# Kernel tuning notes

Measured on AMD Instinct MI355X. Metric: run time of the kernel, lower is better.

The kernel has to match this reference:

```python
import jax, jax.numpy as jnp
import numpy as np

EPS = 1e-5
HEADS, KK, UU, VV, MM = 4, 16, 1, 64, 23
PAD = (MM - 1) // 2


def _bn(x, gamma, beta, mean, var):
    # eval-mode BatchNorm2d over channel axis 1 of (b, c, w, h)
    scale = gamma / jnp.sqrt(var + EPS)
    return (x - mean[:, None, None]) * scale[:, None, None] + beta[:, None, None]


def setup_inputs() -> dict:
    key = jax.random.key(0)
    ks = jax.random.split(key, 13)
    B, C, W, H = 8, 256, 64, 64
    return {
        "x": jax.random.normal(ks[0], (B, C, W, H), jnp.float32),
        "Wq": jax.random.normal(ks[1], (KK * HEADS, C), jnp.float32) * 0.05,
        "q_gamma": jax.random.uniform(ks[2], (KK * HEADS,), jnp.float32),
        "q_beta": jax.random.normal(ks[3], (KK * HEADS,), jnp.float32) * 0.05,
        "q_mean": jax.random.normal(ks[4], (KK * HEADS,), jnp.float32) * 0.05,
        "q_var": jax.random.uniform(ks[5], (KK * HEADS,), jnp.float32) + 0.5,
        "Wk": jax.random.normal(ks[6], (KK * UU, C), jnp.float32) * 0.05,
        "Wv": jax.random.normal(ks[7], (VV * UU, C), jnp.float32) * 0.05,
        "v_gamma": jax.random.uniform(ks[8], (VV * UU,), jnp.float32),
        "v_beta": jax.random.normal(ks[9], (VV * UU,), jnp.float32) * 0.05,
        "v_mean": jax.random.normal(ks[10], (VV * UU,), jnp.float32) * 0.05,
        "v_var": jax.random.uniform(ks[11], (VV * UU,), jnp.float32) + 0.5,
        "embedding": jax.random.normal(ks[12], (KK, UU, 1, MM, MM), jnp.float32),
    }


def reference(x, Wq, q_gamma, q_beta, q_mean, q_var, Wk, Wv, v_gamma, v_beta, v_mean, v_var, embedding):
    b, C, w, h = x.shape
    n = w * h
    # 1x1 conv projections as channel GEMMs
    q = jnp.einsum('bcij,oc->boij', x, Wq)
    q = _bn(q, q_gamma, q_beta, q_mean, q_var).reshape(b, HEADS, KK, n)
    kf = jnp.einsum('bcij,oc->boij', x, Wk).reshape(b, KK, UU, n)
    kf = jax.nn.softmax(kf, axis=-1)  # softmax over spatial positions
    v = jnp.einsum('bcij,oc->boij', x, Wv)
    v = _bn(v, v_gamma, v_beta, v_mean, v_var)  # (b, vv*uu, w, h)
    v_flat = v.reshape(b, VV, UU, n)
    # content lambda
    lambda_c = jnp.einsum('bkum,bvum->bkv', kf, v_flat)
    y_c = jnp.einsum('bhkn,bkv->bhvn', q, lambda_c)
    # positional lambda via depth-1 conv3d over (vv, w, h)
    v5 = v.reshape(b, UU, VV, w, h)
    lambda_p = jax.lax.conv_general_dilated(
        v5, embedding, window_strides=(1, 1, 1),
        padding=[(0, 0), (PAD, PAD), (PAD, PAD)],
        dimension_numbers=('NCDHW', 'OIDHW', 'NCDHW'))  # (b, kk, vv, w, h)
    lambda_p = lambda_p.reshape(b, KK, VV, n)
    y_p = jnp.einsum('bhkn,bkvn->bhvn', q, lambda_p)
    out = (y_c + y_p).reshape(b, HEADS * VV, w, h)
    return out
```

## Files before the change

kernel.cpp:

```cpp
#include <hip/hip_runtime.h>

typedef __attribute__((ext_vector_type(8))) short bf16x8;
typedef __attribute__((ext_vector_type(4))) float f32x4;

#define EPS 1e-5f
#define B 8
#define C 256
#define NPIX 4096
#define NCH 144
#define ROW_V 64
#define ROW_KF 128
#define PAD 11
#define VH_WORDS 3840

#define WP_OFF    0u
#define BIAS_OFF  36864u
#define PROJ_OFF  37120u
#define RMAX_OFF  4755712u
#define RSC_OFF   4755840u
#define LC_OFF    4755968u
#define ET_OFF    4764160u
#define QT_OFF    4811264u
#define OUTT_OFF  6908416u
#define WS_NEED_QT    6908416u
#define WS_NEED_FULL  15297024u

__device__ inline short f2bf(float f) {
  unsigned u = __float_as_uint(f);
  return (short)((u + 0x7fffu + ((u >> 16) & 1u)) >> 16);
}

__global__ __launch_bounds__(256) void k_wfold(
    const float* __restrict__ Wq, const float* __restrict__ qg, const float* __restrict__ qb,
    const float* __restrict__ qm, const float* __restrict__ qv,
    const float* __restrict__ Wk, const float* __restrict__ Wv,
    const float* __restrict__ vg, const float* __restrict__ vb,
    const float* __restrict__ vm, const float* __restrict__ vvar,
    float* __restrict__ Wt, float* __restrict__ biasp) {
  int o = blockIdx.x;
  int t = threadIdx.x;
  const float* src; float s, bias;
  if (o < 64) {
    s = qg[o] * rsqrtf(qv[o] + EPS); bias = qb[o] - qm[o] * s; src = Wq + o * C;
  } else if (o < 128) {
    int i = o - 64;
    s = vg[i] * rsqrtf(vvar[i] + EPS); bias = vb[i] - vm[i] * s; src = Wv + i * C;
  } else {
    int i = o - 128; s = 1.f; bias = 0.f; src = Wk + i * C;
  }
  Wt[t * NCH + o] = src[t] * s;
  if (t == 0) biasp[o] = bias;
}

__global__ __launch_bounds__(256) void k_wprep(
    const float* __restrict__ Wt, ushort* __restrict__ wtA) {
  int i = blockIdx.x * 256 + threadIdx.x;
  int mt = i >> 9;
  int rest = i & 511;
  int kt = rest >> 6;
  int lane = rest & 63;
  int m = mt * 16 + (lane & 15);
  int c0 = kt * 32 + (lane >> 4) * 8;
  ushort* dst = wtA + (size_t)i * 8;
  #pragma unroll
  for (int j = 0; j < 8; j++) {
    float v = Wt[(c0 + j) * NCH + m];
    unsigned u = __float_as_uint(v);
    dst[j] = (ushort)((u + 0x7fffu + ((u >> 16) & 1u)) >> 16);
  }
}

__global__ __launch_bounds__(256) void k_eprep(
    const float* __restrict__ emb, ushort* __restrict__ etw) {
  int i = blockIdx.x * 256 + threadIdx.x;
  int s = i / 11776;
  int r = i % 11776;
  int dy = r / 512;
  int l = (r / 8) % 64;
  int jj = r % 8;
  int f = l & 15, q = l >> 4;
  int dx = q * 8 + jj - s;
  float val = (dx >= 0 && dx < 23) ? emb[f * 529 + dy * 23 + dx] : 0.f;
  unsigned u = __float_as_uint(val);
  etw[i] = (ushort)((u + 0x7fffu + ((u >> 16) & 1u)) >> 16);
}

__global__ __launch_bounds__(256) void k_projm(
    const float* __restrict__ x, const ushort* __restrict__ wtA,
    const float* __restrict__ biasp, float* __restrict__ proj) {
  int ntile = blockIdx.x;
  int b = blockIdx.y;
  int t = threadIdx.x;
  int lane = t & 63, w = t >> 6;
  int px = ntile * 64 + w * 16 + (lane & 15);
  int kq = lane >> 4;
  const float* xb = x + (size_t)b * C * NPIX + px;
  const bf16x8* A = (const bf16x8*)wtA;
  f32x4 acc[9];
  #pragma unroll
  for (int i = 0; i < 9; i++) acc[i] = (f32x4)(0.f);
  #pragma unroll 2
  for (int kt = 0; kt < 8; kt++) {
    int c0 = kt * 32 + kq * 8;
    bf16x8 bb;
    #pragma unroll
    for (int j = 0; j < 8; j++) bb[j] = f2bf(xb[(size_t)(c0 + j) * NPIX]);
    #pragma unroll
    for (int mt = 0; mt < 9; mt++) {
      bf16x8 a = A[(mt * 8 + kt) * 64 + lane];
      acc[mt] = __builtin_amdgcn_mfma_f32_16x16x32_bf16(a, bb, acc[mt], 0, 0, 0);
    }
  }
  float* pb = proj + (size_t)b * NCH * NPIX + px;
  #pragma unroll
  for (int mt = 0; mt < 9; mt++) {
    #pragma unroll
    for (int r = 0; r < 4; r++) {
      int ch = mt * 16 + kq * 4 + r;
      pb[(size_t)ch * NPIX] = acc[mt][r] + biasp[ch];
    }
  }
}

__global__ __launch_bounds__(256) void k_proj(
    const float* __restrict__ x, const float* __restrict__ Wt,
    const float* __restrict__ biasp, float* __restrict__ proj) {
  int tile = blockIdx.x;
  int g = blockIdx.y;
  int b = blockIdx.z;
  int t = threadIdx.x;
  int px = tile * 256 + t;
  const float* xb = x + (size_t)b * C * NPIX + px;
  float acc[18];
  #pragma unroll
  for (int i = 0; i < 18; i++) acc[i] = 0.f;
  #pragma unroll 4
  for (int c = 0; c < C; c++) {
    float xv = xb[(size_t)c * NPIX];
    const float* wrow = Wt + c * NCH + g * 18;
    #pragma unroll
    for (int i = 0; i < 18; i++) acc[i] += xv * wrow[i];
  }
  float* ob = proj + ((size_t)b * NCH + g * 18) * NPIX + px;
  #pragma unroll
  for (int i = 0; i < 18; i++) ob[(size_t)i * NPIX] = acc[i] + biasp[g * 18 + i];
}

__global__ __launch_bounds__(256) void k_qtrans(
    const float* __restrict__ proj, float* __restrict__ qT) {
  int ch = blockIdx.x, b = blockIdx.y, t = threadIdx.x;
  __shared__ float buf[4608];
  const float* src = proj + ((size_t)b * NCH + ch) * NPIX;
  for (int it = 0; it < 16; it++) {
    int p = it * 256 + t;
    buf[p + (p >> 3)] = src[p];
  }
  __syncthreads();
  float* dst = qT + ((size_t)b * 64 + ch) * NPIX;
  for (int it = 0; it < 16; it++) {
    int idx = it * 256 + t;
    int s = idx >> 9, i = idx & 511;
    int p = (i >> 3) * 64 + (i & 7) * 8 + s;
    dst[idx] = buf[p + (p >> 3)];
  }
}

__global__ __launch_bounds__(256) void k_vhalo(
    const float* __restrict__ proj, uint* __restrict__ vhg) {
  int v = blockIdx.x, b = blockIdx.y, t = threadIdx.x;
  const float* vrow = proj + ((size_t)b * NCH + ROW_V + v) * NPIX;
  uint* dst = vhg + (size_t)b * NCH * NPIX + (size_t)v * VH_WORDS;
  for (int p2 = t; p2 < 3784; p2 += 256) {
    int hr = p2 / 44;
    int hc = (p2 % 44) * 2;
    int ir = hr - 11;
    int ic0 = hc - 11, ic1 = hc - 10;
    bool rok = (ir >= 0 && ir < 64);
    float f0 = (rok && ic0 >= 0 && ic0 < 64) ? vrow[ir * 64 + ic0] : 0.f;
    float f1 = (rok && ic1 >= 0 && ic1 < 64) ? vrow[ir * 64 + ic1] : 0.f;
    uint u0 = __float_as_uint(f0), u1 = __float_as_uint(f1);
    uint h0 = (u0 + 0x7fffu + ((u0 >> 16) & 1u)) >> 16;
    uint h1 = (u1 + 0x7fffu + ((u1 >> 16) & 1u)) >> 16;
    dst[p2] = (h0 & 0xffffu) | (h1 << 16);
  }
}

__global__ __launch_bounds__(256) void k_softstat(
    const float* __restrict__ proj, float* __restrict__ rmax, float* __restrict__ rsc) {
  int k = blockIdx.x, b = blockIdx.y, t = threadIdx.x;
  const float* row = proj + ((size_t)b * NCH + ROW_KF + k) * NPIX;
  __shared__ float sd[256];
  float m = -1e30f;
  for (int n = t; n < NPIX; n += 256) m = fmaxf(m, row[n]);
  sd[t] = m; __syncthreads();
  for (int s = 128; s > 0; s >>= 1) { if (t < s) sd[t] = fmaxf(sd[t], sd[t + s]); __syncthreads(); }
  m = sd[0]; __syncthreads();
  float sum = 0.f;
  for (int n = t; n < NPIX; n += 256) sum += __expf(row[n] - m);
  sd[t] = sum; __syncthreads();
  for (int s = 128; s > 0; s >>= 1) { if (t < s) sd[t] += sd[t + s]; __syncthreads(); }
  if (t == 0) { rmax[b * 16 + k] = m; rsc[b * 16 + k] = 1.f / sd[0]; }
}

__global__ __launch_bounds__(256) void k_lambda_c(
    const float* __restrict__ proj, const float* __restrict__ rmax,
    const float* __restrict__ rsc, float* __restrict__ lc) {
  int split = blockIdx.x;
  int b = blockIdx.y;
  int t = threadIdx.x;
  int lane = t & 63, w = t >> 6;
  int kr = lane & 15;
  int half = lane >> 4;
  float m = rmax[b * 16 + kr], sc = rsc[b * 16 + kr];
  const float* kfrow = proj + ((size_t)b * NCH + ROW_KF + kr) * NPIX;
  const float* vrow  = proj + ((size_t)b * NCH + ROW_V + w * 16 + kr) * NPIX;
  f32x4 acc = (f32x4)(0.f);
  #pragma unroll
  for (int c = 0; c < 2; c++) {
    int n0 = split * 64 + c * 32 + half * 8;
    float4 fa0 = *(const float4*)(kfrow + n0);
    float4 fa1 = *(const float4*)(kfrow + n0 + 4);
    float4 fb0 = *(const float4*)(vrow + n0);
    float4 fb1 = *(const float4*)(vrow + n0 + 4);
    bf16x8 a, bb;
    a[0] = f2bf(__expf(fa0.x - m) * sc); a[1] = f2bf(__expf(fa0.y - m) * sc);
    a[2] = f2bf(__expf(fa0.z - m) * sc); a[3] = f2bf(__expf(fa0.w - m) * sc);
    a[4] = f2bf(__expf(fa1.x - m) * sc); a[5] = f2bf(__expf(fa1.y - m) * sc);
    a[6] = f2bf(__expf(fa1.z - m) * sc); a[7] = f2bf(__expf(fa1.w - m) * sc);
    bb[0] = f2bf(fb0.x); bb[1] = f2bf(fb0.y); bb[2] = f2bf(fb0.z); bb[3] = f2bf(fb0.w);
    bb[4] = f2bf(fb1.x); bb[5] = f2bf(fb1.y); bb[6] = f2bf(fb1.z); bb[7] = f2bf(fb1.w);
    acc = __builtin_amdgcn_mfma_f32_16x16x32_bf16(a, bb, acc, 0, 0, 0);
  }
  #pragma unroll
  for (int r = 0; r < 4; r++) {
    int k = half * 4 + r;
    atomicAdd(&lc[((size_t)b * 16 + k) * 64 + w * 16 + kr], acc[r]);
  }
}

__global__ __launch_bounds__(256, 2) void k_conv_mfma(
    const float* __restrict__ proj, const ushort* __restrict__ etw,
    const float* __restrict__ qT, const float* __restrict__ lc,
    const uint* __restrict__ vhg,
    float* __restrict__ outT, float* __restrict__ out, int mode) {
  int s = blockIdx.x;
  int v = blockIdx.y;
  int b = blockIdx.z;
  int t = threadIdx.x;
  __shared__ __align__(16) ushort vh[86 * 88];
  __shared__ __align__(16) ushort elds[23 * 64 * 8];

  {
    const uint4* src = (const uint4*)etw + s * 1472;
    uint4* dst = (uint4*)elds;
    for (int i = t; i < 1472; i += 256) dst[i] = src[i];
  }
  if (mode != 0) {
    const uint4* vsrc = (const uint4*)(vhg + (size_t)b * NCH * NPIX + (size_t)v * VH_WORDS);
    uint4* vdst = (uint4*)vh;
    for (int i = t; i < 946; i += 256) vdst[i] = vsrc[i];
  } else {
    const float* vrow = proj + ((size_t)b * NCH + ROW_V + v) * NPIX;
    for (int i = t; i < 86 * 88; i += 256) {
      int hr = i / 88, hc = i % 88;
      int ir = hr - 11, ic = hc - 11;
      float val = (ir >= 0 && ir < 64 && ic >= 0 && ic < 64) ? vrow[ir * 64 + ic] : 0.f;
      unsigned u = __float_as_uint(val);
      vh[i] = (ushort)((u + 0x7fffu + ((u >> 16) & 1u)) >> 16);
    }
  }
  __syncthreads();

  int lane = t & 63, w = t >> 6;
  int n_ = lane & 15, q = lane >> 4;
  int rn = n_ >> 3, g = n_ & 7;

  f32x4 acc[8];
  #pragma unroll
  for (int i = 0; i < 8; i++) acc[i] = (f32x4)(0.f);

  const bf16x8* vh8 = (const bf16x8*)vh;
  const bf16x8* e8 = (const bf16x8*)elds;
  int baseA = (w * 16 + rn) * 11 + g + q;

  bf16x8 bfr[16];
  #pragma unroll
  for (int r = 0; r < 16; r++)
    bfr[(r & 1) * 8 + ((r >> 1) & 7)] = vh8[baseA + r * 11];

  #pragma unroll
  for (int dy = 0; dy < 23; dy++) {
    bf16x8 ef = e8[dy * 64 + lane];
    bf16x8 tmp;
    if (dy + 16 <= 36) tmp = vh8[baseA + (dy + 16) * 11];
    #pragma unroll
    for (int tt = 0; tt < 8; tt++) {
      int r = dy + 2 * tt;
      acc[tt] = __builtin_amdgcn_mfma_f32_16x16x32_bf16(
          ef, bfr[(r & 1) * 8 + ((r >> 1) & 7)], acc[tt], 0, 0, 0);
    }
    if (dy + 16 <= 36) {
      int rr = dy + 16;
      bfr[(rr & 1) * 8 + ((rr >> 1) & 7)] = tmp;
    }
  }

  float lcv[4];
  #pragma unroll
  for (int r = 0; r < 4; r++) lcv[r] = lc[((size_t)b * 16 + q * 4 + r) * 64 + v];

  if (mode != 0) {
    const float* qTb = qT + (size_t)b * 64 * NPIX;
    float* obT = outT + (size_t)b * 256 * NPIX;
    float* ob = out + (size_t)b * 256 * NPIX;
    #pragma unroll
    for (int tt = 0; tt < 8; tt++) {
      int row = w * 16 + 2 * tt + rn;
      int io = s * 512 + row * 8 + g;
      float lam[4];
      #pragma unroll
      for (int r = 0; r < 4; r++) lam[r] = acc[tt][r] + lcv[r];
      float y[4];
      #pragma unroll
      for (int h = 0; h < 4; h++) {
        float a = 0.f;
        #pragma unroll
        for (int r = 0; r < 4; r++)
          a += qTb[(size_t)(h * 16 + q * 4 + r) * NPIX + io] * lam[r];
        y[h] = a;
      }
      #pragma unroll
      for (int h = 0; h < 4; h++) {
        y[h] += __shfl_xor(y[h], 16);
        y[h] += __shfl_xor(y[h], 32);
      }
      if (q == 0) {
        if (mode == 2) {
          #pragma unroll
          for (int h = 0; h < 4; h++) obT[(size_t)(h * 64 + v) * NPIX + io] = y[h];
        } else {
          int p = row * 64 + 8 * g + s;
          #pragma unroll
          for (int h = 0; h < 4; h++) ob[(size_t)(h * 64 + v) * NPIX + p] = y[h];
        }
      }
    }
  } else {
    const float* qbp = proj + (size_t)b * NCH * NPIX;
    float* ob = out + (size_t)b * 256 * NPIX;
    #pragma unroll
    for (int tt = 0; tt < 8; tt++) {
      int p = (w * 16 + 2 * tt + rn) * 64 + 8 * g + s;
      float lam[4];
      #pragma unroll
      for (int r = 0; r < 4; r++) lam[r] = acc[tt][r] + lcv[r];
      float y[4];
      #pragma unroll
      for (int h = 0; h < 4; h++) {
        float a = 0.f;
        #pragma unroll
        for (int r = 0; r < 4; r++)
          a += qbp[(size_t)(h * 16 + q * 4 + r) * NPIX + p] * lam[r];
        y[h] = a;
      }
      #pragma unroll
      for (int h = 0; h < 4; h++) {
        y[h] += __shfl_xor(y[h], 16);
        y[h] += __shfl_xor(y[h], 32);
      }
      if (q == 0) {
        #pragma unroll
        for (int h = 0; h < 4; h++) ob[(size_t)(h * 64 + v) * NPIX + p] = y[h];
      }
    }
  }
}

__global__ __launch_bounds__(256) void k_outtrans(
    const float* __restrict__ outT, float* __restrict__ out) {
  int ch = blockIdx.x, b = blockIdx.y, t = threadIdx.x;
  __shared__ float buf[4608];
  const float* src = outT + ((size_t)b * 256 + ch) * NPIX;
  for (int it = 0; it < 16; it++) {
    int idx = it * 256 + t;
    int s = idx >> 9, i = idx & 511;
    int p = (i >> 3) * 64 + (i & 7) * 8 + s;
    buf[p + (p >> 3)] = src[idx];
  }
  __syncthreads();
  float* dst = out + ((size_t)b * 256 + ch) * NPIX;
  for (int it = 0; it < 16; it++) {
    int p = it * 256 + t;
    dst[p] = buf[p + (p >> 3)];
  }
}

extern "C" void kernel_launch(void* const* d_in, const int* in_sizes, int n_in,
                              void* d_out, int out_size, void* d_ws, size_t ws_size,
                              hipStream_t stream) {
  const float* x    = (const float*)d_in[0];
  const float* Wq   = (const float*)d_in[1];
  const float* qg   = (const float*)d_in[2];
  const float* qbta = (const float*)d_in[3];
  const float* qm   = (const float*)d_in[4];
  const float* qv   = (const float*)d_in[5];
  const float* Wk   = (const float*)d_in[6];
  const float* Wv   = (const float*)d_in[7];
  const float* vg   = (const float*)d_in[8];
  const float* vb   = (const float*)d_in[9];
  const float* vm   = (const float*)d_in[10];
  const float* vvar = (const float*)d_in[11];
  const float* emb  = (const float*)d_in[12];
  float* ws   = (float*)d_ws;
  float* Wt   = ws + WP_OFF;
  float* bp   = ws + BIAS_OFF;
  float* proj = ws + PROJ_OFF;
  float* rmax = ws + RMAX_OFF;
  float* rsc  = ws + RSC_OFF;
  float* lcw  = ws + LC_OFF;
  ushort* etw = (ushort*)(ws + ET_OFF);
  float* qT   = ws + QT_OFF;
  float* outT = ws + OUTT_OFF;
  float* out  = (float*)d_out;
  uint* vhg   = (uint*)proj;
  ushort* wtA = (ushort*)qT;

  size_t wsf = ws_size / sizeof(float);
  int mode = (wsf >= WS_NEED_FULL) ? 2 : ((wsf >= WS_NEED_QT) ? 1 : 0);

  hipLaunchKernelGGL(k_wfold, dim3(144), dim3(256), 0, stream,
                     Wq, qg, qbta, qm, qv, Wk, Wv, vg, vb, vm, vvar, Wt, bp);
  hipLaunchKernelGGL(k_eprep, dim3(368), dim3(256), 0, stream, emb, etw);
  hipMemsetAsync(lcw, 0, 16 * 64 * B * sizeof(float), stream);
  if (mode >= 1) {
    hipLaunchKernelGGL(k_wprep, dim3(18), dim3(256), 0, stream, Wt, wtA);
    hipLaunchKernelGGL(k_projm, dim3(64, 8), dim3(256), 0, stream, x, wtA, bp, proj);
    hipLaunchKernelGGL(k_qtrans, dim3(64, 8), dim3(256), 0, stream, proj, qT);
    hipLaunchKernelGGL(k_vhalo, dim3(64, 8), dim3(256), 0, stream, proj, vhg);
  } else {
    hipLaunchKernelGGL(k_proj, dim3(16, 8, 8), dim3(256), 0, stream, x, Wt, bp, proj);
  }
  hipLaunchKernelGGL(k_softstat, dim3(16, 8), dim3(256), 0, stream, proj, rmax, rsc);
  hipLaunchKernelGGL(k_lambda_c, dim3(64, 8), dim3(256), 0, stream, proj, rmax, rsc, lcw);
  hipLaunchKernelGGL(k_conv_mfma, dim3(8, 64, 8), dim3(256), 0, stream,
                     proj, etw, qT, lcw, vhg, outT, out, mode);
  if (mode == 2)
    hipLaunchKernelGGL(k_outtrans, dim3(256, 8), dim3(256), 0, stream, outT, out);
}
```

Before: 217.1 us.

## Fuse softmax stats into lambda_c, merge prep kernels, read embedding from global

Drops the separate softmax-statistics kernel. The unnormalized exp is accumulated into lambda_c along with a per-row sum via atomics, and the conv kernel divides by that sum. The weight-fold and embedding-prep kernels are merged into one launch. The conv kernel now reads embedding fragments directly from global memory instead of staging them in LDS, and its occupancy hint is raised to 6. Skipping max-subtraction risks exp overflow for large logits, and the global embedding reads depend on cache hits.

```diff
diff --git a/kernel.cpp b/kernel.cpp
--- a/kernel.cpp
+++ b/kernel.cpp
@@ -17,7 +17,6 @@
 #define BIAS_OFF  36864u
 #define PROJ_OFF  37120u
 #define RMAX_OFF  4755712u
-#define RSC_OFF   4755840u
 #define LC_OFF    4755968u
 #define ET_OFF    4764160u
 #define QT_OFF    4811264u
@@ -30,26 +29,41 @@
   return (short)((u + 0x7fffu + ((u >> 16) & 1u)) >> 16);
 }
 
-__global__ __launch_bounds__(256) void k_wfold(
+__global__ __launch_bounds__(256) void k_prep(
     const float* __restrict__ Wq, const float* __restrict__ qg, const float* __restrict__ qb,
     const float* __restrict__ qm, const float* __restrict__ qv,
     const float* __restrict__ Wk, const float* __restrict__ Wv,
     const float* __restrict__ vg, const float* __restrict__ vb,
     const float* __restrict__ vm, const float* __restrict__ vvar,
-    float* __restrict__ Wt, float* __restrict__ biasp) {
-  int o = blockIdx.x;
+    const float* __restrict__ emb,
+    float* __restrict__ Wt, float* __restrict__ biasp, ushort* __restrict__ etw) {
   int t = threadIdx.x;
-  const float* src; float s, bias;
-  if (o < 64) {
-    s = qg[o] * rsqrtf(qv[o] + EPS); bias = qb[o] - qm[o] * s; src = Wq + o * C;
-  } else if (o < 128) {
-    int i = o - 64;
-    s = vg[i] * rsqrtf(vvar[i] + EPS); bias = vb[i] - vm[i] * s; src = Wv + i * C;
+  if (blockIdx.x < 144) {
+    int o = blockIdx.x;
+    const float* src; float s, bias;
+    if (o < 64) {
+      s = qg[o] * rsqrtf(qv[o] + EPS); bias = qb[o] - qm[o] * s; src = Wq + o * C;
+    } else if (o < 128) {
+      int i = o - 64;
+      s = vg[i] * rsqrtf(vvar[i] + EPS); bias = vb[i] - vm[i] * s; src = Wv + i * C;
+    } else {
+      int i = o - 128; s = 1.f; bias = 0.f; src = Wk + i * C;
+    }
+    Wt[t * NCH + o] = src[t] * s;
+    if (t == 0) biasp[o] = bias;
   } else {
-    int i = o - 128; s = 1.f; bias = 0.f; src = Wk + i * C;
-  }
-  Wt[t * NCH + o] = src[t] * s;
-  if (t == 0) biasp[o] = bias;
+    int i = (blockIdx.x - 144) * 256 + t;
+    int s = i / 11776;
+    int r = i % 11776;
+    int dy = r / 512;
+    int l = (r / 8) % 64;
+    int jj = r % 8;
+    int f = l & 15, q = l >> 4;
+    int dx = q * 8 + jj - s;
+    float val = (dx >= 0 && dx < 23) ? emb[f * 529 + dy * 23 + dx] : 0.f;
+    unsigned u = __float_as_uint(val);
+    etw[i] = (ushort)((u + 0x7fffu + ((u >> 16) & 1u)) >> 16);
+  }
 }
 
 __global__ __launch_bounds__(256) void k_wprep(
@@ -68,21 +82,6 @@
     unsigned u = __float_as_uint(v);
     dst[j] = (ushort)((u + 0x7fffu + ((u >> 16) & 1u)) >> 16);
   }
-}
-
-__global__ __launch_bounds__(256) void k_eprep(
-    const float* __restrict__ emb, ushort* __restrict__ etw) {
-  int i = blockIdx.x * 256 + threadIdx.x;
-  int s = i / 11776;
-  int r = i % 11776;
-  int dy = r / 512;
-  int l = (r / 8) % 64;
-  int jj = r % 8;
-  int f = l & 15, q = l >> 4;
-  int dx = q * 8 + jj - s;
-  float val = (dx >= 0 && dx < 23) ? emb[f * 529 + dy * 23 + dx] : 0.f;
-  unsigned u = __float_as_uint(val);
-  etw[i] = (ushort)((u + 0x7fffu + ((u >> 16) & 1u)) >> 16);
 }
 
 __global__ __launch_bounds__(256) void k_projm(
@@ -185,36 +184,18 @@
   }
 }
 
-__global__ __launch_bounds__(256) void k_softstat(
-    const float* __restrict__ proj, float* __restrict__ rmax, float* __restrict__ rsc) {
-  int k = blockIdx.x, b = blockIdx.y, t = threadIdx.x;
-  const float* row = proj + ((size_t)b * NCH + ROW_KF + k) * NPIX;
-  __shared__ float sd[256];
-  float m = -1e30f;
-  for (int n = t; n < NPIX; n += 256) m = fmaxf(m, row[n]);
-  sd[t] = m; __syncthreads();
-  for (int s = 128; s > 0; s >>= 1) { if (t < s) sd[t] = fmaxf(sd[t], sd[t + s]); __syncthreads(); }
-  m = sd[0]; __syncthreads();
-  float sum = 0.f;
-  for (int n = t; n < NPIX; n += 256) sum += __expf(row[n] - m);
-  sd[t] = sum; __syncthreads();
-  for (int s = 128; s > 0; s >>= 1) { if (t < s) sd[t] += sd[t + s]; __syncthreads(); }
-  if (t == 0) { rmax[b * 16 + k] = m; rsc[b * 16 + k] = 1.f / sd[0]; }
-}
-
 __global__ __launch_bounds__(256) void k_lambda_c(
-    const float* __restrict__ proj, const float* __restrict__ rmax,
-    const float* __restrict__ rsc, float* __restrict__ lc) {
+    const float* __restrict__ proj, float* __restrict__ lc, float* __restrict__ S) {
   int split = blockIdx.x;
   int b = blockIdx.y;
   int t = threadIdx.x;
   int lane = t & 63, w = t >> 6;
   int kr = lane & 15;
   int half = lane >> 4;
-  float m = rmax[b * 16 + kr], sc = rsc[b * 16 + kr];
   const float* kfrow = proj + ((size_t)b * NCH + ROW_KF + kr) * NPIX;
   const float* vrow  = proj + ((size_t)b * NCH + ROW_V + w * 16 + kr) * NPIX;
   f32x4 acc = (f32x4)(0.f);
+  float ssum = 0.f;
   #pragma unroll
   for (int c = 0; c < 2; c++) {
     int n0 = split * 64 + c * 32 + half * 8;
@@ -222,11 +203,12 @@
     float4 fa1 = *(const float4*)(kfrow + n0 + 4);
     float4 fb0 = *(const float4*)(vrow + n0);
     float4 fb1 = *(const float4*)(vrow + n0 + 4);
+    float e0 = __expf(fa0.x), e1 = __expf(fa0.y), e2 = __expf(fa0.z), e3 = __expf(fa0.w);
+    float e4 = __expf(fa1.x), e5 = __expf(fa1.y), e6 = __expf(fa1.z), e7 = __expf(fa1.w);
+    ssum += (e0 + e1 + e2 + e3) + (e4 + e5 + e6 + e7);
     bf16x8 a, bb;
-    a[0] = f2bf(__expf(fa0.x - m) * sc); a[1] = f2bf(__expf(fa0.y - m) * sc);
-    a[2] = f2bf(__expf(fa0.z - m) * sc); a[3] = f2bf(__expf(fa0.w - m) * sc);
-    a[4] = f2bf(__expf(fa1.x - m) * sc); a[5] = f2bf(__expf(fa1.y - m) * sc);
-    a[6] = f2bf(__expf(fa1.z - m) * sc); a[7] = f2bf(__expf(fa1.w - m) * sc);
+    a[0] = f2bf(e0); a[1] = f2bf(e1); a[2] = f2bf(e2); a[3] = f2bf(e3);
+    a[4] = f2bf(e4); a[5] = f2bf(e5); a[6] = f2bf(e6); a[7] = f2bf(e7);
     bb[0] = f2bf(fb0.x); bb[1] = f2bf(fb0.y); bb[2] = f2bf(fb0.z); bb[3] = f2bf(fb0.w);
     bb[4] = f2bf(fb1.x); bb[5] = f2bf(fb1.y); bb[6] = f2bf(fb1.z); bb[7] = f2bf(fb1.w);
     acc = __builtin_amdgcn_mfma_f32_16x16x32_bf16(a, bb, acc, 0, 0, 0);
@@ -236,25 +218,24 @@
     int k = half * 4 + r;
     atomicAdd(&lc[((size_t)b * 16 + k) * 64 + w * 16 + kr], acc[r]);
   }
-}
-
-__global__ __launch_bounds__(256, 2) void k_conv_mfma(
+  if (w == 0) {
+    ssum += __shfl_xor(ssum, 16);
+    ssum += __shfl_xor(ssum, 32);
+    if (lane < 16) atomicAdd(&S[b * 16 + kr], ssum);
+  }
+}
+
+__global__ __launch_bounds__(256, 6) void k_conv_mfma(
     const float* __restrict__ proj, const ushort* __restrict__ etw,
     const float* __restrict__ qT, const float* __restrict__ lc,
-    const uint* __restrict__ vhg,
+    const float* __restrict__ S, const uint* __restrict__ vhg,
     float* __restrict__ outT, float* __restrict__ out, int mode) {
   int s = blockIdx.x;
   int v = blockIdx.y;
   int b = blockIdx.z;
   int t = threadIdx.x;
   __shared__ __align__(16) ushort vh[86 * 88];
-  __shared__ __align__(16) ushort elds[23 * 64 * 8];
-
-  {
-    const uint4* src = (const uint4*)etw + s * 1472;
-    uint4* dst = (uint4*)elds;
-    for (int i = t; i < 1472; i += 256) dst[i] = src[i];
-  }
+
   if (mode != 0) {
     const uint4* vsrc = (const uint4*)(vhg + (size_t)b * NCH * NPIX + (size_t)v * VH_WORDS);
     uint4* vdst = (uint4*)vh;
@@ -280,7 +261,7 @@
   for (int i = 0; i < 8; i++) acc[i] = (f32x4)(0.f);
 
   const bf16x8* vh8 = (const bf16x8*)vh;
-  const bf16x8* e8 = (const bf16x8*)elds;
+  const bf16x8* e8 = (const bf16x8*)etw + (size_t)s * 1472;
   int baseA = (w * 16 + rn) * 11 + g + q;
 
   bf16x8 bfr[16];
@@ -307,7 +288,10 @@
 
   float lcv[4];
   #pragma unroll
-  for (int r = 0; r < 4; r++) lcv[r] = lc[((size_t)b * 16 + q * 4 + r) * 64 + v];
+  for (int r = 0; r < 4; r++) {
+    int k = q * 4 + r;
+    lcv[r] = lc[((size_t)b * 16 + k) * 64 + v] / S[b * 16 + k];
+  }
 
   if (mode != 0) {
     const float* qTb = qT + (size_t)b * 64 * NPIX;
@@ -415,8 +399,7 @@
   float* Wt   = ws + WP_OFF;
   float* bp   = ws + BIAS_OFF;
   float* proj = ws + PROJ_OFF;
-  float* rmax = ws + RMAX_OFF;
-  float* rsc  = ws + RSC_OFF;
+  float* Sw   = ws + RMAX_OFF;
   float* lcw  = ws + LC_OFF;
   ushort* etw = (ushort*)(ws + ET_OFF);
   float* qT   = ws + QT_OFF;
@@ -428,10 +411,9 @@
   size_t wsf = ws_size / sizeof(float);
   int mode = (wsf >= WS_NEED_FULL) ? 2 : ((wsf >= WS_NEED_QT) ? 1 : 0);
 
-  hipLaunchKernelGGL(k_wfold, dim3(144), dim3(256), 0, stream,
-                     Wq, qg, qbta, qm, qv, Wk, Wv, vg, vb, vm, vvar, Wt, bp);
-  hipLaunchKernelGGL(k_eprep, dim3(368), dim3(256), 0, stream, emb, etw);
-  hipMemsetAsync(lcw, 0, 16 * 64 * B * sizeof(float), stream);
+  hipLaunchKernelGGL(k_prep, dim3(512), dim3(256), 0, stream,
+                     Wq, qg, qbta, qm, qv, Wk, Wv, vg, vb, vm, vvar, emb, Wt, bp, etw);
+  hipMemsetAsync(Sw, 0, 8448 * sizeof(float), stream);
   if (mode >= 1) {
     hipLaunchKernelGGL(k_wprep, dim3(18), dim3(256), 0, stream, Wt, wtA);
     hipLaunchKernelGGL(k_projm, dim3(64, 8), dim3(256), 0, stream, x, wtA, bp, proj);
@@ -440,10 +422,9 @@
   } else {
     hipLaunchKernelGGL(k_proj, dim3(16, 8, 8), dim3(256), 0, stream, x, Wt, bp, proj);
   }
-  hipLaunchKernelGGL(k_softstat, dim3(16, 8), dim3(256), 0, stream, proj, rmax, rsc);
-  hipLaunchKernelGGL(k_lambda_c, dim3(64, 8), dim3(256), 0, stream, proj, rmax, rsc, lcw);
+  hipLaunchKernelGGL(k_lambda_c, dim3(64, 8), dim3(256), 0, stream, proj, lcw, Sw);
   hipLaunchKernelGGL(k_conv_mfma, dim3(8, 64, 8), dim3(256), 0, stream,
-                     proj, etw, qT, lcw, vhg, outT, out, mode);
+                     proj, etw, qT, lcw, Sw, vhg, outT, out, mode);
   if (mode == 2)
     hipLaunchKernelGGL(k_outtrans, dim3(256, 8), dim3(256), 0, stream, outT, out);
 }
```

After: 559.3 us. 158% more time.
